# Kernel optimization log

Hardware: AMD Instinct MI355X
Metric: run time of the kernel (lower is better)

## Reference

```python
import jax, jax.numpy as jnp
import numpy as np

EMBED_DIM = 1024
NUM_HEADS = 16
HEAD_DIM = EMBED_DIM // NUM_HEADS
BATCH = 1  # module's torch.t(torch.squeeze(k)) requires batch==1
SEQ = 2048


def setup_inputs() -> dict:
    key = jax.random.key(0)
    k1, k2, k3, k4, k5 = jax.random.split(key, 5)
    s = 1.0 / np.sqrt(EMBED_DIM)
    return {
        "qkv": jax.random.normal(k1, (BATCH, SEQ, EMBED_DIM), jnp.float32),
        "w_in": jax.random.normal(k2, (EMBED_DIM, 3 * EMBED_DIM), jnp.float32) * s,
        "b_in": jax.random.normal(k3, (3 * EMBED_DIM,), jnp.float32) * 0.01,
        "w_out": jax.random.normal(k4, (EMBED_DIM, EMBED_DIM), jnp.float32) * s,
        "b_out": jax.random.normal(k5, (EMBED_DIM,), jnp.float32) * 0.01,
    }


def reference(qkv, w_in, b_in, w_out, b_out):
    B, S, E = qkv.shape
    H, D = NUM_HEADS, HEAD_DIM
    proj = qkv @ w_in + b_in                      # [B,S,3E]
    q, k, v = jnp.split(proj, 3, axis=2)          # each [B,S,E]
    q = q.reshape(B, S, H, D)
    k = k.reshape(B, S, H, D)
    v = v.reshape(B, S, H, D)
    scale = 1.0 / np.sqrt(D).astype(np.float32)
    scores = jnp.einsum("bshd,bthd->bhst", q, k) * scale  # [B,H,S,S]
    attn = jax.nn.softmax(scores, axis=-1)
    out = jnp.einsum("bhst,bthd->bshd", attn, v).reshape(B, S, E)
    return out @ w_out + b_out
```

## Files before the change

kernel.cpp:

```cpp
#include <hip/hip_runtime.h>
#include <math.h>

typedef short bf16x8 __attribute__((ext_vector_type(8)));
typedef _Float16 f16x8 __attribute__((ext_vector_type(8)));
typedef _Float16 f16x4 __attribute__((ext_vector_type(4)));
typedef float f32x4 __attribute__((ext_vector_type(4)));
typedef unsigned short u16x4 __attribute__((ext_vector_type(4)));

#define S_LEN 2048
#define E_DIM 1024
#define H_NUM 16
#define D_DIM 64
#define LDP   (3 * E_DIM)
#define QSCALE 0.18033688011112042f

#define MFMA16(a, b, c)  __builtin_amdgcn_mfma_f32_16x16x32_bf16((a), (b), (c), 0, 0, 0)
#define MFMA16H(a, b, c) __builtin_amdgcn_mfma_f32_16x16x32_f16((a), (b), (c), 0, 0, 0)

__device__ __forceinline__ unsigned short f2bf(float f) {
    union { float f; unsigned int u; } v; v.f = f;
    unsigned int r = v.u + 0x7FFFu + ((v.u >> 16) & 1u);
    return (unsigned short)(r >> 16);
}
__device__ __forceinline__ float exp2_fast(float x) {
    float r; asm("v_exp_f32 %0, %1" : "=v"(r) : "v"(x)); return r;
}
__device__ __forceinline__ unsigned int cvt_pk_bf16(float lo, float hi) {
    unsigned int r;
    asm("v_cvt_pk_bf16_f32 %0, %1, %2" : "=v"(r) : "v"(lo), "v"(hi));
    return r;
}
__device__ __forceinline__ void gl_lds16(const void* g, unsigned short* l) {
    __builtin_amdgcn_global_load_lds(
        (const __attribute__((address_space(1))) void*)g,
        (__attribute__((address_space(3))) void*)l, 16, 0, 0);
}

__global__ __launch_bounds__(256) void prep_kernel(
    const float* __restrict__ qkv, _Float16* __restrict__ Ah,
    const float* __restrict__ w_in, _Float16* __restrict__ Wt1,
    const float* __restrict__ w_out, _Float16* __restrict__ Wt2)
{
    __shared__ float tile[64][65];
    const int bid = blockIdx.x;
    const int t = threadIdx.x;

    if (bid < 2048) {
        const int i = bid * 256 + t;
        const float4 v = ((const float4*)qkv)[i];
        f16x4 hh;
        hh[0] = (_Float16)v.x; hh[1] = (_Float16)v.y;
        hh[2] = (_Float16)v.z; hh[3] = (_Float16)v.w;
        ((f16x4*)Ah)[i] = hh;
        return;
    }
    const float* B;
    _Float16* Bt;
    int bx, by, N;
    if (bid < 2816) { B = w_in;  Bt = Wt1; N = 3 * E_DIM; bx = (bid - 2048) % 48; by = (bid - 2048) / 48; }
    else            { B = w_out; Bt = Wt2; N = E_DIM;     bx = (bid - 2816) % 16; by = (bid - 2816) / 16; }
    const int K = E_DIM;
    const int k0 = by * 64, n0 = bx * 64;
    const int r4 = t >> 6, c = t & 63;
#pragma unroll
    for (int rep = 0; rep < 16; ++rep)
        tile[rep * 4 + r4][c] = B[(size_t)(k0 + rep * 4 + r4) * N + n0 + c];
    __syncthreads();
#pragma unroll
    for (int rep = 0; rep < 16; ++rep) {
        const int n = rep * 4 + r4;
        Bt[(size_t)(n0 + n) * K + k0 + c] = (_Float16)tile[c][n];
    }
}

template <int BM, int BN, int OUT_MODE, int TWO_PASS>
__global__ __launch_bounds__(256) void gemm_f16_kernel(
    const _Float16* __restrict__ Ah, const _Float16* __restrict__ Al,
    const _Float16* __restrict__ Bt, const float* __restrict__ bias,
    void* __restrict__ Cout, int M, int N, int K, int nbx)
{
    constexpr int AROWS = TWO_PASS ? 2 * BM : BM;
    constexpr int ROWS = AROWS + BN;
    constexpr int EPW  = ROWS / 64;
    constexpr int MI = BM / 32, NI = BN / 32;
    __shared__ unsigned short lds[2 * ROWS * 32];

    const int nwg = gridDim.x;
    const int bid = blockIdx.x;
    const int qch = nwg >> 3;
    const int swz = (bid & 7) * qch + (bid >> 3);
    const int n0 = (swz % nbx) * BN;
    const int m0 = (swz / nbx) * BM;

    const int t = threadIdx.x;
    const int wid = t >> 6, lane = t & 63;
    const int wr = wid >> 1, wc = wid & 1;
    const int lc = lane & 15, g = lane >> 4;
    const int lrow = lane >> 2;
    const int lcol = (lane & 3) * 8;

    f32x4 acc[MI][NI];
    const f32x4 zf = {0.f, 0.f, 0.f, 0.f};
#pragma unroll
    for (int mi = 0; mi < MI; ++mi)
#pragma unroll
        for (int ni = 0; ni < NI; ++ni) acc[mi][ni] = zf;

    auto stage = [&](int k0, int b) {
        unsigned short* base = &lds[b * ROWS * 32];
#pragma unroll
        for (int e = 0; e < EPW; ++e) {
            const int rb = (wid * EPW + e) * 16;
            const int rr = rb + lrow;
            const _Float16* gp;
            if (rb < BM)                            gp = &Ah[(size_t)(m0 + rr) * K + k0 + lcol];
            else if (TWO_PASS && rb < 2 * BM)       gp = &Al[(size_t)(m0 + rr - BM) * K + k0 + lcol];
            else                                    gp = &Bt[(size_t)(n0 + rr - AROWS) * K + k0 + lcol];
            gl_lds16(gp, base + rb * 32);
        }
    };

    stage(0, 0);
    const int NK = K / 32;
    for (int ks = 0; ks < NK; ++ks) {
        __syncthreads();
        if (ks + 1 < NK) stage((ks + 1) * 32, (ks + 1) & 1);
        const unsigned short* cb = &lds[(ks & 1) * ROWS * 32];

        f16x8 bfr[NI];
#pragma unroll
        for (int ni = 0; ni < NI; ++ni)
            bfr[ni] = *(const f16x8*)&cb[(AROWS + wc * (BN / 2) + ni * 16 + lc) * 32 + g * 8];
#pragma unroll
        for (int mi = 0; mi < MI; ++mi) {
            const int ar = wr * (BM / 2) + mi * 16 + lc;
            const f16x8 ah = *(const f16x8*)&cb[ar * 32 + g * 8];
#pragma unroll
            for (int ni = 0; ni < NI; ++ni)
                acc[mi][ni] = MFMA16H(ah, bfr[ni], acc[mi][ni]);
            if (TWO_PASS) {
                const f16x8 al = *(const f16x8*)&cb[(BM + ar) * 32 + g * 8];
#pragma unroll
                for (int ni = 0; ni < NI; ++ni)
                    acc[mi][ni] = MFMA16H(al, bfr[ni], acc[mi][ni]);
            }
        }
    }

#pragma unroll
    for (int ni = 0; ni < NI; ++ni) {
        const int col = n0 + wc * (BN / 2) + ni * 16 + lc;
        const float bv = bias[col];
        float sc = 1.f;
        if (OUT_MODE == 1) sc = (col < E_DIM) ? QSCALE : 1.f;
#pragma unroll
        for (int mi = 0; mi < MI; ++mi) {
            const int rbase = m0 + wr * (BM / 2) + mi * 16 + g * 4;
#pragma unroll
            for (int i = 0; i < 4; ++i) {
                const float v = acc[mi][ni][i] + bv;
                if (OUT_MODE == 1)
                    ((unsigned short*)Cout)[(size_t)(rbase + i) * N + col] = f2bf(v * sc);
                else
                    ((float*)Cout)[(size_t)(rbase + i) * N + col] = v;
            }
        }
    }
}

__global__ __launch_bounds__(512, 4) void attn_mfma_kernel(
    const unsigned short* __restrict__ proj,
    _Float16* __restrict__ Oh, _Float16* __restrict__ Ol)
{
    __shared__ unsigned short lds[20480];
    float* ldsf = (float*)lds;
    const int Q_OFF = 16384;

    const int t = threadIdx.x;
    const int w = t >> 6, lane = t & 63;
    const int lc = lane & 15, g = lane >> 4;
    const int qg = w & 3;
    const int half = w >> 2;
    const int ts = t & 255;

    const int bid = blockIdx.x;
    const int swb = (bid & 7) * 64 + (bid >> 3);
    const int qt = swb & 31;
    const int h  = swb >> 5;
    const int q0 = qt * 64;

    const size_t qoff = (size_t)h * D_DIM;
    const size_t koff = E_DIM + (size_t)h * D_DIM;
    const size_t voff = 2 * E_DIM + (size_t)h * D_DIM;

    const int KO = half * 4096;
    const int VO = 8192 + half * 4096;
    const int kvbase = half * (S_LEN / 2);

    const int r  = ts >> 2;
    const int s  = (ts & 3) * 16;
    const int sw = (r & 7) << 3;
    const int kv = (ts & 15) * 4;
    const int d0 = (ts >> 4) * 4;

    uint4 ka, kb;
    u16x4 vr[4];
    auto load_kv = [&](int tile) {
        const int t0 = kvbase + tile * 64;
        const unsigned short* gk = &proj[(size_t)(t0 + r) * LDP + koff + s];
        ka = ((const uint4*)gk)[0];
        kb = ((const uint4*)gk)[1];
#pragma unroll
        for (int r2 = 0; r2 < 4; ++r2)
            vr[r2] = *(const u16x4*)&proj[(size_t)(t0 + kv + r2) * LDP + voff + d0];
    };
    auto store_kv = [&]() {
        *(uint4*)&lds[KO + r * 64 + (s ^ sw)]       = ka;
        *(uint4*)&lds[KO + r * 64 + ((s + 8) ^ sw)] = kb;
#pragma unroll
        for (int j = 0; j < 4; ++j) {
            u16x4 w4; w4[0] = vr[0][j]; w4[1] = vr[1][j]; w4[2] = vr[2][j]; w4[3] = vr[3][j];
            const int d = d0 + j;
            *(u16x4*)&lds[VO + d * 64 + (kv ^ ((d & 7) << 3))] = w4;
        }
    };

    if (half == 0) {
        const unsigned short* gq = &proj[(size_t)(q0 + r) * LDP + qoff + s];
        const uint4 v0 = ((const uint4*)gq)[0];
        const uint4 v1 = ((const uint4*)gq)[1];
        *(uint4*)&lds[Q_OFF + r * 64 + (s ^ sw)]       = v0;
        *(uint4*)&lds[Q_OFF + r * 64 + ((s + 8) ^ sw)] = v1;
    }
    load_kv(0);
    store_kv();
    __syncthreads();

    bf16x8 qB0, qB1;
    {
        const int rq = qg * 16 + lc;
        const int swq = (rq & 7) << 3;
        qB0 = *(const bf16x8*)&lds[Q_OFF + rq * 64 + ((g * 8) ^ swq)];
        qB1 = *(const bf16x8*)&lds[Q_OFF + rq * 64 + ((32 + g * 8) ^ swq)];
    }
    __syncthreads();

    f32x4 oacc[4];
    const f32x4 zf = {0.f, 0.f, 0.f, 0.f};
#pragma unroll
    for (int i = 0; i < 4; ++i) oacc[i] = zf;
    float mrun = -1e30f;
    float lsum = 0.f;

    const int pb = Q_OFF + w * 512 + lc * 32;
    const int psw = ((lc >> 1) & 3) << 3;

    const int NTH = (S_LEN / 2) / 64;
    for (int tt = 0; tt < NTH; ++tt) {
        if (tt + 1 < NTH) load_kv(tt + 1);

        f32x4 sacc[4];
#pragma unroll
        for (int c = 0; c < 4; ++c) sacc[c] = zf;
        __builtin_amdgcn_s_setprio(1);
#pragma unroll
        for (int c = 0; c < 4; ++c) {
            const int kr = c * 16 + lc;
            const int swk = (kr & 7) << 3;
            const bf16x8 kf = *(const bf16x8*)&lds[KO + kr * 64 + ((g * 8) ^ swk)];
            sacc[c] = MFMA16(kf, qB0, sacc[c]);
        }
#pragma unroll
        for (int c = 0; c < 4; ++c) {
            const int kr = c * 16 + lc;
            const int swk = (kr & 7) << 3;
            const bf16x8 kf = *(const bf16x8*)&lds[KO + kr * 64 + ((32 + g * 8) ^ swk)];
            sacc[c] = MFMA16(kf, qB1, sacc[c]);
        }
        __builtin_amdgcn_s_setprio(0);

        float lmax = fmaxf(fmaxf(sacc[0][0], sacc[0][1]), fmaxf(sacc[0][2], sacc[0][3]));
        lmax = fmaxf(lmax, fmaxf(fmaxf(sacc[1][0], sacc[1][1]), fmaxf(sacc[1][2], sacc[1][3])));
        lmax = fmaxf(lmax, fmaxf(fmaxf(sacc[2][0], sacc[2][1]), fmaxf(sacc[2][2], sacc[2][3])));
        lmax = fmaxf(lmax, fmaxf(fmaxf(sacc[3][0], sacc[3][1]), fmaxf(sacc[3][2], sacc[3][3])));
        if (__any(lmax > mrun + 8.0f)) {
            float mx = lmax;
            mx = fmaxf(mx, __shfl_xor(mx, 16));
            mx = fmaxf(mx, __shfl_xor(mx, 32));
            const float mnew = fmaxf(mrun, mx);
            const float fs = exp2_fast(mrun - mnew);
            lsum *= fs;
            mrun = mnew;
#pragma unroll
            for (int i = 0; i < 4; ++i) {
                const float fsi = __shfl(fs, 4 * g + i, 16);
                oacc[0][i] *= fsi; oacc[1][i] *= fsi;
                oacc[2][i] *= fsi; oacc[3][i] *= fsi;
            }
        }

#pragma unroll
        for (int c = 0; c < 4; ++c)
#pragma unroll
            for (int i = 0; i < 4; ++i)
                sacc[c][i] = exp2_fast(sacc[c][i] - mrun);
        lsum += ((sacc[0][0] + sacc[0][1]) + (sacc[0][2] + sacc[0][3]))
              + ((sacc[1][0] + sacc[1][1]) + (sacc[1][2] + sacc[1][3]))
              + ((sacc[2][0] + sacc[2][1]) + (sacc[2][2] + sacc[2][3]))
              + ((sacc[3][0] + sacc[3][1]) + (sacc[3][2] + sacc[3][3]));

#pragma unroll
        for (int hf = 0; hf < 2; ++hf) {
#pragma unroll
            for (int c2 = 0; c2 < 2; ++c2) {
                const int c = hf * 2 + c2;
                uint2 w2;
                w2.x = cvt_pk_bf16(sacc[c][0], sacc[c][1]);
                w2.y = cvt_pk_bf16(sacc[c][2], sacc[c][3]);
                *(uint2*)&lds[pb + ((c2 * 16 + 4 * g) ^ psw)] = w2;
            }
            const bf16x8 pA = *(const bf16x8*)&lds[pb + ((g * 8) ^ psw)];
            __builtin_amdgcn_s_setprio(1);
#pragma unroll
            for (int dt = 0; dt < 4; ++dt) {
                const int vrow = dt * 16 + lc;
                const int swv = (vrow & 7) << 3;
                const bf16x8 vB = *(const bf16x8*)&lds[VO + vrow * 64 + ((hf * 32 + g * 8) ^ swv)];
                oacc[dt] = MFMA16(pA, vB, oacc[dt]);
            }
            __builtin_amdgcn_s_setprio(0);
        }

        __syncthreads();
        if (tt + 1 < NTH) {
            store_kv();
            __syncthreads();
        }
    }

    float ps = lsum;
    ps += __shfl_xor(ps, 16);
    ps += __shfl_xor(ps, 32);

    if (half == 1) {
#pragma unroll
        for (int dt = 0; dt < 4; ++dt)
#pragma unroll
            for (int i = 0; i < 4; ++i)
                ldsf[qg * 1024 + (dt * 4 + i) * 64 + lane] = oacc[dt][i];
        ldsf[4096 + qg * 128 + lane] = mrun;
        ldsf[4096 + qg * 128 + 64 + lane] = ps;
    }
    __syncthreads();
    if (half == 0) {
        const float m2 = ldsf[4096 + qg * 128 + lane];
        const float l2 = ldsf[4096 + qg * 128 + 64 + lane];
        const float mf = fmaxf(mrun, m2);
        const float f1 = exp2_fast(mrun - mf);
        const float f2 = exp2_fast(m2 - mf);
        const float inv = 1.f / (ps * f1 + l2 * f2);
#pragma unroll
        for (int i = 0; i < 4; ++i) {
            const float f1i = __shfl(f1, 4 * g + i, 16);
            const float f2i = __shfl(f2, 4 * g + i, 16);
            const float invi = __shfl(inv, 4 * g + i, 16);
            const int row = q0 + qg * 16 + 4 * g + i;
#pragma unroll
            for (int dt = 0; dt < 4; ++dt) {
                const float o2 = ldsf[qg * 1024 + (dt * 4 + i) * 64 + lane];
                const float x = (oacc[dt][i] * f1i + o2 * f2i) * invi;
                const _Float16 xh = (_Float16)x;
                const _Float16 xl = (_Float16)(x - (float)xh);
                const size_t off = (size_t)row * E_DIM + h * D_DIM + dt * 16 + lc;
                Oh[off] = xh;
                Ol[off] = xl;
            }
        }
    }
}

extern "C" void kernel_launch(void* const* d_in, const int* in_sizes, int n_in,
                              void* d_out, int out_size, void* d_ws, size_t ws_size,
                              hipStream_t stream)
{
    (void)in_sizes; (void)n_in; (void)out_size; (void)ws_size;

    const float* qkv   = (const float*)d_in[0];
    const float* w_in  = (const float*)d_in[1];
    const float* b_in  = (const float*)d_in[2];
    const float* w_out = (const float*)d_in[3];
    const float* b_out = (const float*)d_in[4];
    float* out = (float*)d_out;

    unsigned char* ws = (unsigned char*)d_ws;
    _Float16* Wt1 = (_Float16*)(ws);
    _Float16* Wt2 = (_Float16*)(ws + 6291456);
    _Float16* Ah1 = (_Float16*)(ws + 8388608);
    _Float16* Al1 = (_Float16*)(ws + 12582912);
    unsigned short* proj = (unsigned short*)(ws + 16777216);
    _Float16* Oh = Ah1;
    _Float16* Ol = Al1;

    prep_kernel<<<3072, 256, 0, stream>>>(qkv, Ah1, w_in, Wt1, w_out, Wt2);

    gemm_f16_kernel<128, 128, 1, 0><<<384, 256, 0, stream>>>(
        Ah1, Ah1, Wt1, b_in, (void*)proj, S_LEN, 3 * E_DIM, E_DIM, 24);

    attn_mfma_kernel<<<512, 512, 0, stream>>>(proj, Oh, Ol);

    gemm_f16_kernel<64, 64, 0, 1><<<512, 256, 0, stream>>>(
        Oh, Ol, Wt2, b_out, (void*)out, S_LEN, E_DIM, E_DIM, 16);
}
```

Before: 90.43 us.

## Split attention KV across four wave groups with 32-row tiles; drop split-f16 output

The attention kernel now handles 32 query rows per block, and the KV sequence is split four ways across wave pairs. It uses 32-wide KV tiles and merges the four partial softmax states at the end. The grid doubles to 1024 blocks to improve occupancy and parallelism. The attention output is written only as a single f16 buffer, so the output GEMM runs single-pass instead of hi/lo two-pass, which removes half of its A traffic at some cost in precision. The QKV GEMM tile changes to 128x96 with 512 blocks, and staging is generalized to handle row counts that are not a multiple of 64.

```diff
diff --git a/kernel.cpp b/kernel.cpp
--- a/kernel.cpp
+++ b/kernel.cpp
@@ -81,7 +81,7 @@
 {
     constexpr int AROWS = TWO_PASS ? 2 * BM : BM;
     constexpr int ROWS = AROWS + BN;
-    constexpr int EPW  = ROWS / 64;
+    constexpr int NISS = ROWS / 16;
     constexpr int MI = BM / 32, NI = BN / 32;
     __shared__ unsigned short lds[2 * ROWS * 32];
 
@@ -109,8 +109,8 @@
     auto stage = [&](int k0, int b) {
         unsigned short* base = &lds[b * ROWS * 32];
 #pragma unroll
-        for (int e = 0; e < EPW; ++e) {
-            const int rb = (wid * EPW + e) * 16;
+        for (int e = wid; e < NISS; e += 4) {
+            const int rb = e * 16;
             const int rr = rb + lrow;
             const _Float16* gp;
             if (rb < BM)                            gp = &Ah[(size_t)(m0 + rr) * K + k0 + lcol];
@@ -169,44 +169,43 @@
 }
 
 __global__ __launch_bounds__(512, 4) void attn_mfma_kernel(
-    const unsigned short* __restrict__ proj,
-    _Float16* __restrict__ Oh, _Float16* __restrict__ Ol)
+    const unsigned short* __restrict__ proj, _Float16* __restrict__ Oh)
 {
     __shared__ unsigned short lds[20480];
     float* ldsf = (float*)lds;
-    const int Q_OFF = 16384;
 
     const int t = threadIdx.x;
     const int w = t >> 6, lane = t & 63;
     const int lc = lane & 15, g = lane >> 4;
-    const int qg = w & 3;
-    const int half = w >> 2;
-    const int ts = t & 255;
+    const int qg = w & 1;
+    const int qq = w >> 1;
+    const int ts = t & 127;
 
     const int bid = blockIdx.x;
-    const int swb = (bid & 7) * 64 + (bid >> 3);
-    const int qt = swb & 31;
-    const int h  = swb >> 5;
-    const int q0 = qt * 64;
+    const int swb = (bid & 7) * 128 + (bid >> 3);
+    const int qt = swb & 63;
+    const int h  = swb >> 6;
+    const int q0 = qt * 32;
 
     const size_t qoff = (size_t)h * D_DIM;
     const size_t koff = E_DIM + (size_t)h * D_DIM;
     const size_t voff = 2 * E_DIM + (size_t)h * D_DIM;
 
-    const int KO = half * 4096;
-    const int VO = 8192 + half * 4096;
-    const int kvbase = half * (S_LEN / 2);
+    const int KO = qq * 2048;
+    const int VO = 8192 + qq * 2048;
+    const int P_OFF = 16384;
+    const int kvbase = qq * 512;
 
     const int r  = ts >> 2;
     const int s  = (ts & 3) * 16;
     const int sw = (r & 7) << 3;
-    const int kv = (ts & 15) * 4;
-    const int d0 = (ts >> 4) * 4;
+    const int kv = (ts & 7) * 4;
+    const int d0 = (ts >> 3) * 4;
 
     uint4 ka, kb;
     u16x4 vr[4];
     auto load_kv = [&](int tile) {
-        const int t0 = kvbase + tile * 64;
+        const int t0 = kvbase + tile * 32;
         const unsigned short* gk = &proj[(size_t)(t0 + r) * LDP + koff + s];
         ka = ((const uint4*)gk)[0];
         kb = ((const uint4*)gk)[1];
@@ -221,16 +220,16 @@
         for (int j = 0; j < 4; ++j) {
             u16x4 w4; w4[0] = vr[0][j]; w4[1] = vr[1][j]; w4[2] = vr[2][j]; w4[3] = vr[3][j];
             const int d = d0 + j;
-            *(u16x4*)&lds[VO + d * 64 + (kv ^ ((d & 7) << 3))] = w4;
+            *(u16x4*)&lds[VO + d * 32 + (kv ^ ((d & 3) << 3))] = w4;
         }
     };
 
-    if (half == 0) {
+    if (t < 128) {
         const unsigned short* gq = &proj[(size_t)(q0 + r) * LDP + qoff + s];
         const uint4 v0 = ((const uint4*)gq)[0];
         const uint4 v1 = ((const uint4*)gq)[1];
-        *(uint4*)&lds[Q_OFF + r * 64 + (s ^ sw)]       = v0;
-        *(uint4*)&lds[Q_OFF + r * 64 + ((s + 8) ^ sw)] = v1;
+        *(uint4*)&lds[P_OFF + r * 64 + (s ^ sw)]       = v0;
+        *(uint4*)&lds[P_OFF + r * 64 + ((s + 8) ^ sw)] = v1;
     }
     load_kv(0);
     store_kv();
@@ -240,8 +239,8 @@
     {
         const int rq = qg * 16 + lc;
         const int swq = (rq & 7) << 3;
-        qB0 = *(const bf16x8*)&lds[Q_OFF + rq * 64 + ((g * 8) ^ swq)];
-        qB1 = *(const bf16x8*)&lds[Q_OFF + rq * 64 + ((32 + g * 8) ^ swq)];
+        qB0 = *(const bf16x8*)&lds[P_OFF + rq * 64 + ((g * 8) ^ swq)];
+        qB1 = *(const bf16x8*)&lds[P_OFF + rq * 64 + ((32 + g * 8) ^ swq)];
     }
     __syncthreads();
 
@@ -252,37 +251,29 @@
     float mrun = -1e30f;
     float lsum = 0.f;
 
-    const int pb = Q_OFF + w * 512 + lc * 32;
-    const int psw = ((lc >> 1) & 3) << 3;
-
-    const int NTH = (S_LEN / 2) / 64;
+    const int pb = P_OFF + w * 512 + lc * 32;
+    const int psw = (lc & 3) << 3;
+
+    const int NTH = 512 / 32;
     for (int tt = 0; tt < NTH; ++tt) {
         if (tt + 1 < NTH) load_kv(tt + 1);
 
-        f32x4 sacc[4];
-#pragma unroll
-        for (int c = 0; c < 4; ++c) sacc[c] = zf;
+        f32x4 sacc[2];
+        sacc[0] = zf; sacc[1] = zf;
         __builtin_amdgcn_s_setprio(1);
 #pragma unroll
-        for (int c = 0; c < 4; ++c) {
+        for (int c = 0; c < 2; ++c) {
             const int kr = c * 16 + lc;
             const int swk = (kr & 7) << 3;
-            const bf16x8 kf = *(const bf16x8*)&lds[KO + kr * 64 + ((g * 8) ^ swk)];
-            sacc[c] = MFMA16(kf, qB0, sacc[c]);
-        }
-#pragma unroll
-        for (int c = 0; c < 4; ++c) {
-            const int kr = c * 16 + lc;
-            const int swk = (kr & 7) << 3;
-            const bf16x8 kf = *(const bf16x8*)&lds[KO + kr * 64 + ((32 + g * 8) ^ swk)];
-            sacc[c] = MFMA16(kf, qB1, sacc[c]);
+            const bf16x8 kf0 = *(const bf16x8*)&lds[KO + kr * 64 + ((g * 8) ^ swk)];
+            const bf16x8 kf1 = *(const bf16x8*)&lds[KO + kr * 64 + ((32 + g * 8) ^ swk)];
+            sacc[c] = MFMA16(kf0, qB0, sacc[c]);
+            sacc[c] = MFMA16(kf1, qB1, sacc[c]);
         }
         __builtin_amdgcn_s_setprio(0);
 
         float lmax = fmaxf(fmaxf(sacc[0][0], sacc[0][1]), fmaxf(sacc[0][2], sacc[0][3]));
         lmax = fmaxf(lmax, fmaxf(fmaxf(sacc[1][0], sacc[1][1]), fmaxf(sacc[1][2], sacc[1][3])));
-        lmax = fmaxf(lmax, fmaxf(fmaxf(sacc[2][0], sacc[2][1]), fmaxf(sacc[2][2], sacc[2][3])));
-        lmax = fmaxf(lmax, fmaxf(fmaxf(sacc[3][0], sacc[3][1]), fmaxf(sacc[3][2], sacc[3][3])));
         if (__any(lmax > mrun + 8.0f)) {
             float mx = lmax;
             mx = fmaxf(mx, __shfl_xor(mx, 16));
@@ -300,36 +291,29 @@
         }
 
 #pragma unroll
-        for (int c = 0; c < 4; ++c)
+        for (int c = 0; c < 2; ++c)
 #pragma unroll
             for (int i = 0; i < 4; ++i)
                 sacc[c][i] = exp2_fast(sacc[c][i] - mrun);
         lsum += ((sacc[0][0] + sacc[0][1]) + (sacc[0][2] + sacc[0][3]))
-              + ((sacc[1][0] + sacc[1][1]) + (sacc[1][2] + sacc[1][3]))
-              + ((sacc[2][0] + sacc[2][1]) + (sacc[2][2] + sacc[2][3]))
-              + ((sacc[3][0] + sacc[3][1]) + (sacc[3][2] + sacc[3][3]));
-
-#pragma unroll
-        for (int hf = 0; hf < 2; ++hf) {
-#pragma unroll
-            for (int c2 = 0; c2 < 2; ++c2) {
-                const int c = hf * 2 + c2;
-                uint2 w2;
-                w2.x = cvt_pk_bf16(sacc[c][0], sacc[c][1]);
-                w2.y = cvt_pk_bf16(sacc[c][2], sacc[c][3]);
-                *(uint2*)&lds[pb + ((c2 * 16 + 4 * g) ^ psw)] = w2;
-            }
-            const bf16x8 pA = *(const bf16x8*)&lds[pb + ((g * 8) ^ psw)];
-            __builtin_amdgcn_s_setprio(1);
-#pragma unroll
-            for (int dt = 0; dt < 4; ++dt) {
-                const int vrow = dt * 16 + lc;
-                const int swv = (vrow & 7) << 3;
-                const bf16x8 vB = *(const bf16x8*)&lds[VO + vrow * 64 + ((hf * 32 + g * 8) ^ swv)];
-                oacc[dt] = MFMA16(pA, vB, oacc[dt]);
-            }
-            __builtin_amdgcn_s_setprio(0);
-        }
+              + ((sacc[1][0] + sacc[1][1]) + (sacc[1][2] + sacc[1][3]));
+
+#pragma unroll
+        for (int c = 0; c < 2; ++c) {
+            uint2 w2;
+            w2.x = cvt_pk_bf16(sacc[c][0], sacc[c][1]);
+            w2.y = cvt_pk_bf16(sacc[c][2], sacc[c][3]);
+            *(uint2*)&lds[pb + ((c * 16 + 4 * g) ^ psw)] = w2;
+        }
+        const bf16x8 pA = *(const bf16x8*)&lds[pb + ((g * 8) ^ psw)];
+        __builtin_amdgcn_s_setprio(1);
+#pragma unroll
+        for (int dt = 0; dt < 4; ++dt) {
+            const int vrow = dt * 16 + lc;
+            const bf16x8 vB = *(const bf16x8*)&lds[VO + vrow * 32 + ((g * 8) ^ ((lc & 3) << 3))];
+            oacc[dt] = MFMA16(pA, vB, oacc[dt]);
+        }
+        __builtin_amdgcn_s_setprio(0);
 
         __syncthreads();
         if (tt + 1 < NTH) {
@@ -342,38 +326,47 @@
     ps += __shfl_xor(ps, 16);
     ps += __shfl_xor(ps, 32);
 
-    if (half == 1) {
+    if (qq > 0) {
+        const int base = (w - 2) * 1024;
 #pragma unroll
         for (int dt = 0; dt < 4; ++dt)
 #pragma unroll
             for (int i = 0; i < 4; ++i)
-                ldsf[qg * 1024 + (dt * 4 + i) * 64 + lane] = oacc[dt][i];
-        ldsf[4096 + qg * 128 + lane] = mrun;
-        ldsf[4096 + qg * 128 + 64 + lane] = ps;
+                ldsf[base + (dt * 4 + i) * 64 + lane] = oacc[dt][i];
+        ldsf[6144 + (w - 2) * 128 + lane] = mrun;
+        ldsf[6144 + (w - 2) * 128 + 64 + lane] = ps;
     }
     __syncthreads();
-    if (half == 0) {
-        const float m2 = ldsf[4096 + qg * 128 + lane];
-        const float l2 = ldsf[4096 + qg * 128 + 64 + lane];
-        const float mf = fmaxf(mrun, m2);
-        const float f1 = exp2_fast(mrun - mf);
-        const float f2 = exp2_fast(m2 - mf);
-        const float inv = 1.f / (ps * f1 + l2 * f2);
+    if (qq == 0) {
+        float mm[3], ll[3];
+#pragma unroll
+        for (int j = 0; j < 3; ++j) {
+            const int idx = (qg + 2 * j) * 128;
+            mm[j] = ldsf[6144 + idx + lane];
+            ll[j] = ldsf[6144 + idx + 64 + lane];
+        }
+        float mf = fmaxf(fmaxf(mrun, mm[0]), fmaxf(mm[1], mm[2]));
+        const float f0 = exp2_fast(mrun - mf);
+        float fj[3];
+#pragma unroll
+        for (int j = 0; j < 3; ++j) fj[j] = exp2_fast(mm[j] - mf);
+        const float L = f0 * ps + fj[0] * ll[0] + fj[1] * ll[1] + fj[2] * ll[2];
+        const float inv = 1.f / L;
 #pragma unroll
         for (int i = 0; i < 4; ++i) {
-            const float f1i = __shfl(f1, 4 * g + i, 16);
-            const float f2i = __shfl(f2, 4 * g + i, 16);
+            const float f0i = __shfl(f0, 4 * g + i, 16);
+            const float f1i = __shfl(fj[0], 4 * g + i, 16);
+            const float f2i = __shfl(fj[1], 4 * g + i, 16);
+            const float f3i = __shfl(fj[2], 4 * g + i, 16);
             const float invi = __shfl(inv, 4 * g + i, 16);
             const int row = q0 + qg * 16 + 4 * g + i;
 #pragma unroll
             for (int dt = 0; dt < 4; ++dt) {
-                const float o2 = ldsf[qg * 1024 + (dt * 4 + i) * 64 + lane];
-                const float x = (oacc[dt][i] * f1i + o2 * f2i) * invi;
-                const _Float16 xh = (_Float16)x;
-                const _Float16 xl = (_Float16)(x - (float)xh);
-                const size_t off = (size_t)row * E_DIM + h * D_DIM + dt * 16 + lc;
-                Oh[off] = xh;
-                Ol[off] = xl;
+                float x = oacc[dt][i] * f0i;
+                x += ldsf[(qg + 0) * 1024 + (dt * 4 + i) * 64 + lane] * f1i;
+                x += ldsf[(qg + 2) * 1024 + (dt * 4 + i) * 64 + lane] * f2i;
+                x += ldsf[(qg + 4) * 1024 + (dt * 4 + i) * 64 + lane] * f3i;
+                Oh[(size_t)row * E_DIM + h * D_DIM + dt * 16 + lc] = (_Float16)(x * invi);
             }
         }
     }
@@ -396,18 +389,16 @@
     _Float16* Wt1 = (_Float16*)(ws);
     _Float16* Wt2 = (_Float16*)(ws + 6291456);
     _Float16* Ah1 = (_Float16*)(ws + 8388608);
-    _Float16* Al1 = (_Float16*)(ws + 12582912);
     unsigned short* proj = (unsigned short*)(ws + 16777216);
     _Float16* Oh = Ah1;
-    _Float16* Ol = Al1;
 
     prep_kernel<<<3072, 256, 0, stream>>>(qkv, Ah1, w_in, Wt1, w_out, Wt2);
 
-    gemm_f16_kernel<128, 128, 1, 0><<<384, 256, 0, stream>>>(
-        Ah1, Ah1, Wt1, b_in, (void*)proj, S_LEN, 3 * E_DIM, E_DIM, 24);
-
-    attn_mfma_kernel<<<512, 512, 0, stream>>>(proj, Oh, Ol);
-
-    gemm_f16_kernel<64, 64, 0, 1><<<512, 256, 0, stream>>>(
-        Oh, Ol, Wt2, b_out, (void*)out, S_LEN, E_DIM, E_DIM, 16);
-}
+    gemm_f16_kernel<128, 96, 1, 0><<<512, 256, 0, stream>>>(
+        Ah1, Ah1, Wt1, b_in, (void*)proj, S_LEN, 3 * E_DIM, E_DIM, 32);
+
+    attn_mfma_kernel<<<1024, 512, 0, stream>>>(proj, Oh);
+
+    gemm_f16_kernel<64, 64, 0, 0><<<512, 256, 0, stream>>>(
+        Oh, Oh, Wt2, b_out, (void*)out, S_LEN, E_DIM, E_DIM, 16);
+}
```

New measurement: 116.4 us. 1.29x slower.
